# Kernel optimization log

Measured on AMD Instinct MI355X. Metric: run time of the kernel, lower is better.

## Reference

```python
import jax, jax.numpy as jnp
import numpy as np

KERNEL_SIZE = 3
IGNORE_INDEX = -100


def _unfold(x, k):
    """nn.Unfold(kernel_size=k), stride=1, no padding.
    x: (n, c, h, w) -> (n, c, k*k, L) with L=(h-k+1)*(w-k+1),
    kernel positions in row-major order (matches torch)."""
    n, c, h, w = x.shape
    hp, wp = h - k + 1, w - k + 1
    patches = jnp.stack(
        [x[:, :, i:i + hp, j:j + wp] for i in range(k) for j in range(k)],
        axis=2)  # (n, c, k*k, hp, wp)
    return patches.reshape(n, c, k * k, hp * wp)


def setup_inputs() -> dict:
    key = jax.random.key(0)
    k1, k2 = jax.random.split(key)
    logits = jax.random.normal(k1, (2, 19, 384, 384), dtype=jnp.float32)
    labels = jax.random.randint(k2, (2, 384, 384), 0, 19, dtype=jnp.int32)
    return {"logits": logits, "labels": labels}


def reference(logits, labels):
    n, c, h, w = logits.shape
    # convert_to_one_hot with ignore_index -> zero vector at ignored pixels
    valid = (labels != IGNORE_INDEX)
    oh = jax.nn.one_hot(jnp.where(valid, labels, 0), c, dtype=logits.dtype)
    oh = oh * valid[..., None].astype(logits.dtype)
    oh = jnp.transpose(oh, (0, 3, 1, 2))  # (n, c, h, w)

    lu = _unfold(logits, KERNEL_SIZE)  # (n, c, 9, L)
    yu = _unfold(oh, KERNEL_SIZE)      # (n, c, 9, L)

    aff_map = jnp.einsum('ncal,ncbl->nabl', lu, lu)  # pairwise logit affinity
    lb_map = jnp.einsum('ncal,ncbl->nabl', yu, yu)   # pairwise label affinity

    # BCEWithLogitsLoss(reduction='mean'), numerically stable form
    x, y = aff_map, lb_map
    loss = jnp.mean(jnp.maximum(x, 0) - x * y + jnp.log1p(jnp.exp(-jnp.abs(x))))
    return loss
```

## Files before the change

### kernel.cpp

```cpp
#include <hip/hip_runtime.h>


#define IGNORE_INDEX (-100)

constexpr int Hh = 384, Ww = 384, Cc = 19;
constexpr int HW = Hh * Ww;
constexpr int HP = 382, WP = 382;
constexpr int TX = 32, TY = 8;
constexpr int NT = TX * TY;
constexpr int LXX = TX + 4;
constexpr int LYY = TY + 2;
constexpr int CS  = 20;
constexpr int NBX = Ww / TX, NBY = Hh / TY;
constexpr int NBLK = NBX * NBY * 2;

__device__ __forceinline__ int mult_y(int y, int di) {
    int lo = y - (HP - 1); if (lo < 0) lo = 0;
    int hi = 2 - di;       if (y < hi) hi = y;
    int c = hi - lo + 1;   return c > 0 ? c : 0;
}
__device__ __forceinline__ int mult_x(int x, int dj) {
    int lo = (-dj > 0) ? -dj : 0;
    int lo2 = x - (WP - 1); if (lo2 > lo) lo = lo2;
    int hi = (2 - dj < 2) ? (2 - dj) : 2;
    if (x < hi) hi = x;
    int c = hi - lo + 1;   return c > 0 ? c : 0;
}

__device__ __forceinline__ float softplus(float t) {
    float e = __builtin_amdgcn_exp2f(-1.4426950408889634f * fabsf(t));
    float l = __builtin_amdgcn_logf(1.0f + e);
    return fmaxf(t, 0.0f) + 0.6931471805599453f * l;
}

__global__ __launch_bounds__(NT, 4) void aff_loss_kernel(
        const float* __restrict__ logits, const int* __restrict__ labels,
        double* __restrict__ partial) {
    __shared__ __align__(16) float sv[LYY * LXX * CS];
    __shared__ int   sl[LYY * LXX];
    __shared__ float sred[NT / 64];

    const int n   = blockIdx.z;
    const int tx0 = blockIdx.x * TX;
    const int ty0 = blockIdx.y * TY;
    const int tid = threadIdx.x;
    const int bid = (blockIdx.z * NBY + blockIdx.y) * NBX + blockIdx.x;

    const float* img = logits + (size_t)n * Cc * HW;
    const int*   lab = labels + (size_t)n * HW;

    for (int idx = tid; idx < LYY * LXX; idx += NT) {
        int r = idx / LXX, col = idx - r * LXX;
        int gy = ty0 + r;       if (gy > Hh - 1) gy = Hh - 1;
        int gx = tx0 + col - 2; if (gx < 0) gx = 0; if (gx > Ww - 1) gx = Ww - 1;
        sl[idx] = lab[gy * Ww + gx];
        const float* s = img + gy * Ww + gx;
        float4 t0, t1, t2, t3, t4;
        t0.x = s[0 * HW];  t0.y = s[1 * HW];  t0.z = s[2 * HW];  t0.w = s[3 * HW];
        t1.x = s[4 * HW];  t1.y = s[5 * HW];  t1.z = s[6 * HW];  t1.w = s[7 * HW];
        t2.x = s[8 * HW];  t2.y = s[9 * HW];  t2.z = s[10 * HW]; t2.w = s[11 * HW];
        t3.x = s[12 * HW]; t3.y = s[13 * HW]; t3.z = s[14 * HW]; t3.w = s[15 * HW];
        t4.x = s[16 * HW]; t4.y = s[17 * HW]; t4.z = s[18 * HW]; t4.w = 0.0f;
        float4* dst = reinterpret_cast<float4*>(&sv[idx * CS]);
        dst[0] = t0; dst[1] = t1; dst[2] = t2; dst[3] = t3; dst[4] = t4;
    }
    __syncthreads();

    const int tx = tid & (TX - 1), ty = tid >> 5;
    const int x = tx0 + tx, y = ty0 + ty;
    const int ep = ty * LXX + (tx + 2);

    const float4* P = reinterpret_cast<const float4*>(&sv[ep * CS]);
    const float4 p0 = P[0], p1 = P[1], p2 = P[2], p3 = P[3], p4 = P[4];
    const int lp = sl[ep];
    const bool vp = (lp != IGNORE_INDEX);

    float myf[3], mxf[5];
    #pragma unroll
    for (int i = 0; i < 3; ++i) myf[i] = (float)mult_y(y, i);
    #pragma unroll
    for (int j = 0; j < 5; ++j) mxf[j] = (float)mult_x(x, j - 2);

    auto dot19 = [&](float4 b0, float4 b1, float4 b2, float4 b3, float4 b4) {
        float xa = p0.x * b0.x, xb = p0.y * b0.y;
        xa = fmaf(p0.z, b0.z, xa); xb = fmaf(p0.w, b0.w, xb);
        xa = fmaf(p1.x, b1.x, xa); xb = fmaf(p1.y, b1.y, xb);
        xa = fmaf(p1.z, b1.z, xa); xb = fmaf(p1.w, b1.w, xb);
        xa = fmaf(p2.x, b2.x, xa); xb = fmaf(p2.y, b2.y, xb);
        xa = fmaf(p2.z, b2.z, xa); xb = fmaf(p2.w, b2.w, xb);
        xa = fmaf(p3.x, b3.x, xa); xb = fmaf(p3.y, b3.y, xb);
        xa = fmaf(p3.z, b3.z, xa); xb = fmaf(p3.w, b3.w, xb);
        xa = fmaf(p4.x, b4.x, xa); xb = fmaf(p4.y, b4.y, xb);
        xa = fmaf(p4.z, b4.z, xa);
        return xa + xb;
    };

    float tsum;
    {
        float xd = dot19(p0, p1, p2, p3, p4);
        float t = vp ? -xd : xd;
        tsum = (myf[0] * mxf[2]) * softplus(t);
    }

    const int DY[12] = {0, 0, 1, 1, 1, 1, 1, 2, 2, 2, 2, 2};
    const int DX[12] = {1, 2, -2, -1, 0, 1, 2, -2, -1, 0, 1, 2};
    #pragma unroll
    for (int dd = 0; dd < 12; dd += 2) {
        const int dy0 = DY[dd], dx0 = DX[dd];
        const int dy1 = DY[dd + 1], dx1 = DX[dd + 1];
        const int eq0 = (ty + dy0) * LXX + (tx + 2 + dx0);
        const int eq1 = (ty + dy1) * LXX + (tx + 2 + dx1);
        const float4* Q0 = reinterpret_cast<const float4*>(&sv[eq0 * CS]);
        const float4* Q1 = reinterpret_cast<const float4*>(&sv[eq1 * CS]);
        float4 a0 = Q0[0], a1 = Q0[1], a2 = Q0[2], a3 = Q0[3], a4 = Q0[4];
        float4 c0 = Q1[0], c1 = Q1[1], c2 = Q1[2], c3 = Q1[3], c4 = Q1[4];
        const int lq0 = sl[eq0], lq1 = sl[eq1];
        const float x0 = dot19(a0, a1, a2, a3, a4);
        const float x1 = dot19(c0, c1, c2, c3, c4);
        const float t0 = (vp && lq0 == lp) ? -x0 : x0;
        const float t1 = (vp && lq1 == lp) ? -x1 : x1;
        const float w0 = 2.0f * myf[dy0] * mxf[dx0 + 2];
        const float w1 = 2.0f * myf[dy1] * mxf[dx1 + 2];
        tsum = fmaf(w0, softplus(t0), tsum);
        tsum = fmaf(w1, softplus(t1), tsum);
    }

    for (int off = 32; off > 0; off >>= 1) tsum += __shfl_down(tsum, off, 64);
    const int wid = tid >> 6;
    if ((tid & 63) == 0) sred[wid] = tsum;
    __syncthreads();
    if (tid == 0) {
        double s = 0.0;
        #pragma unroll
        for (int i = 0; i < NT / 64; ++i) s += (double)sred[i];
        partial[bid] = s;
    }
}

__global__ __launch_bounds__(256) void finalize_kernel(
        const double* __restrict__ partial, float* __restrict__ out) {
    __shared__ double sred[4];
    const int tid = threadIdx.x;
    double s = 0.0;
    for (int i = tid; i < NBLK; i += 256) s += partial[i];
    for (int off = 32; off > 0; off >>= 1) s += __shfl_down(s, off, 64);
    if ((tid & 63) == 0) sred[tid >> 6] = s;
    __syncthreads();
    if (tid == 0) {
        double tot = sred[0] + sred[1] + sred[2] + sred[3];
        out[0] = (float)(tot * (1.0 / 23639688.0));
    }
}

extern "C" void kernel_launch(void* const* d_in, const int* in_sizes, int n_in,
                              void* d_out, int out_size, void* d_ws, size_t ws_size,
                              hipStream_t stream) {
    const float* logits = (const float*)d_in[0];
    const int*   labels = (const int*)d_in[1];
    float* out = (float*)d_out;
    double* partial = (double*)d_ws;

    dim3 grid(NBX, NBY, 2);
    aff_loss_kernel<<<grid, NT, 0, stream>>>(logits, labels, partial);
    finalize_kernel<<<1, 256, 0, stream>>>(partial, out);
}
```

Measured before the change: 80.38 us.

## Repack logits into pixel-major channel-padded layout before affinity loss

Adds a repack kernel that transposes the NCHW logits through shared memory into a pixel-major layout with 20 floats per pixel in workspace. The main kernel then loads each halo pixel with five float4 reads instead of nineteen strided scalar loads. The cost is an extra pass that reads the logits and writes a larger intermediate buffer, plus a third kernel launch. It also folds the factor of two into the column multiplicity weights.

Result: slower. 89.03 us (+10.8%).

```diff
diff --git a/kernel.cpp b/kernel.cpp
--- a/kernel.cpp
+++ b/kernel.cpp
@@ -13,6 +13,9 @@
 constexpr int CS  = 20;
 constexpr int NBX = Ww / TX, NBY = Hh / TY;
 constexpr int NBLK = NBX * NBY * 2;
+
+constexpr int AY = 4, AX = 64;
+constexpr int ACS = 21;
 
 __device__ __forceinline__ int mult_y(int y, int di) {
     int lo = y - (HP - 1); if (lo < 0) lo = 0;
@@ -33,8 +36,41 @@
     return fmaxf(t, 0.0f) + 0.6931471805599453f * l;
 }
 
+__global__ __launch_bounds__(256) void repack_kernel(
+        const float* __restrict__ logits, float* __restrict__ rp) {
+    __shared__ float sA[AY * AX * ACS];
+    const int n  = blockIdx.z;
+    const int y0 = blockIdx.y * AY;
+    const int x0 = blockIdx.x * AX;
+    const int tid = threadIdx.x;
+    const float* img = logits + (size_t)n * Cc * HW;
+
+    for (int task = tid; task < Cc * AY * 16; task += 256) {
+        const int c = task >> 6;
+        const int j = task & 63;
+        const int row = j >> 4, seg = j & 15;
+        const float4 v = *reinterpret_cast<const float4*>(
+            img + ((size_t)c * Hh + (y0 + row)) * Ww + x0 + seg * 4);
+        float* d = &sA[((row * AX) + seg * 4) * ACS + c];
+        d[0 * ACS] = v.x; d[1 * ACS] = v.y; d[2 * ACS] = v.z; d[3 * ACS] = v.w;
+    }
+    __syncthreads();
+
+    const int row = tid >> 6, sx = tid & 63;
+    const float* sp = &sA[(row * AX + sx) * ACS];
+    float4 t0, t1, t2, t3, t4;
+    t0.x = sp[0];  t0.y = sp[1];  t0.z = sp[2];  t0.w = sp[3];
+    t1.x = sp[4];  t1.y = sp[5];  t1.z = sp[6];  t1.w = sp[7];
+    t2.x = sp[8];  t2.y = sp[9];  t2.z = sp[10]; t2.w = sp[11];
+    t3.x = sp[12]; t3.y = sp[13]; t3.z = sp[14]; t3.w = sp[15];
+    t4.x = sp[16]; t4.y = sp[17]; t4.z = sp[18]; t4.w = 0.0f;
+    float4* dst = reinterpret_cast<float4*>(
+        rp + ((size_t)n * HW + (size_t)(y0 + row) * Ww + (x0 + sx)) * CS);
+    dst[0] = t0; dst[1] = t1; dst[2] = t2; dst[3] = t3; dst[4] = t4;
+}
+
 __global__ __launch_bounds__(NT, 4) void aff_loss_kernel(
-        const float* __restrict__ logits, const int* __restrict__ labels,
+        const float* __restrict__ rp, const int* __restrict__ labels,
         double* __restrict__ partial) {
     __shared__ __align__(16) float sv[LYY * LXX * CS];
     __shared__ int   sl[LYY * LXX];
@@ -46,7 +82,7 @@
     const int tid = threadIdx.x;
     const int bid = (blockIdx.z * NBY + blockIdx.y) * NBX + blockIdx.x;
 
-    const float* img = logits + (size_t)n * Cc * HW;
+    const float* src = rp + (size_t)n * HW * CS;
     const int*   lab = labels + (size_t)n * HW;
 
     for (int idx = tid; idx < LYY * LXX; idx += NT) {
@@ -54,15 +90,10 @@
         int gy = ty0 + r;       if (gy > Hh - 1) gy = Hh - 1;
         int gx = tx0 + col - 2; if (gx < 0) gx = 0; if (gx > Ww - 1) gx = Ww - 1;
         sl[idx] = lab[gy * Ww + gx];
-        const float* s = img + gy * Ww + gx;
-        float4 t0, t1, t2, t3, t4;
-        t0.x = s[0 * HW];  t0.y = s[1 * HW];  t0.z = s[2 * HW];  t0.w = s[3 * HW];
-        t1.x = s[4 * HW];  t1.y = s[5 * HW];  t1.z = s[6 * HW];  t1.w = s[7 * HW];
-        t2.x = s[8 * HW];  t2.y = s[9 * HW];  t2.z = s[10 * HW]; t2.w = s[11 * HW];
-        t3.x = s[12 * HW]; t3.y = s[13 * HW]; t3.z = s[14 * HW]; t3.w = s[15 * HW];
-        t4.x = s[16 * HW]; t4.y = s[17 * HW]; t4.z = s[18 * HW]; t4.w = 0.0f;
+        const float4* s = reinterpret_cast<const float4*>(
+            src + ((size_t)gy * Ww + gx) * CS);
         float4* dst = reinterpret_cast<float4*>(&sv[idx * CS]);
-        dst[0] = t0; dst[1] = t1; dst[2] = t2; dst[3] = t3; dst[4] = t4;
+        dst[0] = s[0]; dst[1] = s[1]; dst[2] = s[2]; dst[3] = s[3]; dst[4] = s[4];
     }
     __syncthreads();
 
@@ -75,11 +106,11 @@
     const int lp = sl[ep];
     const bool vp = (lp != IGNORE_INDEX);
 
-    float myf[3], mxf[5];
+    float myf[3], mxf2[5];
     #pragma unroll
     for (int i = 0; i < 3; ++i) myf[i] = (float)mult_y(y, i);
     #pragma unroll
-    for (int j = 0; j < 5; ++j) mxf[j] = (float)mult_x(x, j - 2);
+    for (int j = 0; j < 5; ++j) mxf2[j] = 2.0f * (float)mult_x(x, j - 2);
 
     auto dot19 = [&](float4 b0, float4 b1, float4 b2, float4 b3, float4 b4) {
         float xa = p0.x * b0.x, xb = p0.y * b0.y;
@@ -99,7 +130,7 @@
     {
         float xd = dot19(p0, p1, p2, p3, p4);
         float t = vp ? -xd : xd;
-        tsum = (myf[0] * mxf[2]) * softplus(t);
+        tsum = (0.5f * myf[0] * mxf2[2]) * softplus(t);
     }
 
     const int DY[12] = {0, 0, 1, 1, 1, 1, 1, 2, 2, 2, 2, 2};
@@ -119,15 +150,12 @@
         const float x1 = dot19(c0, c1, c2, c3, c4);
         const float t0 = (vp && lq0 == lp) ? -x0 : x0;
         const float t1 = (vp && lq1 == lp) ? -x1 : x1;
-        const float w0 = 2.0f * myf[dy0] * mxf[dx0 + 2];
-        const float w1 = 2.0f * myf[dy1] * mxf[dx1 + 2];
-        tsum = fmaf(w0, softplus(t0), tsum);
-        tsum = fmaf(w1, softplus(t1), tsum);
+        tsum = fmaf(myf[dy0] * mxf2[dx0 + 2], softplus(t0), tsum);
+        tsum = fmaf(myf[dy1] * mxf2[dx1 + 2], softplus(t1), tsum);
     }
 
     for (int off = 32; off > 0; off >>= 1) tsum += __shfl_down(tsum, off, 64);
-    const int wid = tid >> 6;
-    if ((tid & 63) == 0) sred[wid] = tsum;
+    if ((tid & 63) == 0) sred[tid >> 6] = tsum;
     __syncthreads();
     if (tid == 0) {
         double s = 0.0;
@@ -158,9 +186,14 @@
     const float* logits = (const float*)d_in[0];
     const int*   labels = (const int*)d_in[1];
     float* out = (float*)d_out;
-    double* partial = (double*)d_ws;
+    float* rp = (float*)d_ws;
+    double* partial = (double*)((char*)d_ws + (32u << 20));
 
-    dim3 grid(NBX, NBY, 2);
-    aff_loss_kernel<<<grid, NT, 0, stream>>>(logits, labels, partial);
+    dim3 gridA(Ww / AX, Hh / AY, 2);
+    repack_kernel<<<gridA, 256, 0, stream>>>(logits, rp);
+
+    dim3 gridB(NBX, NBY, 2);
+    aff_loss_kernel<<<gridB, NT, 0, stream>>>(rp, labels, partial);
+
     finalize_kernel<<<1, 256, 0, stream>>>(partial, out);
 }
```

## Process both batch images per block with register-prefetched second tile

Applied to the files above, without the earlier changes.

Each block now handles the same spatial tile for both batch images. The second image's halo is loaded into registers while the first tile is computed, so global-load latency overlaps with compute. The grid is flattened and remapped with an XCD-style swizzle of block indices, and the factor of 2 is folded into the x weights. The grid shrinks by half, and each thread holds 40 extra registers for prefetch, which may reduce occupancy.

Result: faster. 74.79 us (-7.0%).

```diff
diff --git a/kernel.cpp b/kernel.cpp
--- a/kernel.cpp
+++ b/kernel.cpp
@@ -10,9 +10,10 @@
 constexpr int NT = TX * TY;
 constexpr int LXX = TX + 4;
 constexpr int LYY = TY + 2;
+constexpr int NE  = LYY * LXX;
 constexpr int CS  = 20;
 constexpr int NBX = Ww / TX, NBY = Hh / TY;
-constexpr int NBLK = NBX * NBY * 2;
+constexpr int NBLK = NBX * NBY;
 
 __device__ __forceinline__ int mult_y(int y, int di) {
     int lo = y - (HP - 1); if (lo < 0) lo = 0;
@@ -36,98 +37,123 @@
 __global__ __launch_bounds__(NT, 4) void aff_loss_kernel(
         const float* __restrict__ logits, const int* __restrict__ labels,
         double* __restrict__ partial) {
-    __shared__ __align__(16) float sv[LYY * LXX * CS];
-    __shared__ int   sl[LYY * LXX];
+    __shared__ __align__(16) float sv[NE * CS];
+    __shared__ int   sl[NE];
     __shared__ float sred[NT / 64];
 
-    const int n   = blockIdx.z;
-    const int tx0 = blockIdx.x * TX;
-    const int ty0 = blockIdx.y * TY;
+    const int bid = ((int)blockIdx.x & 7) * (NBLK / 8) + ((int)blockIdx.x >> 3);
+    const int bx = bid % NBX, by = bid / NBX;
+    const int tx0 = bx * TX, ty0 = by * TY;
     const int tid = threadIdx.x;
-    const int bid = (blockIdx.z * NBY + blockIdx.y) * NBX + blockIdx.x;
-
-    const float* img = logits + (size_t)n * Cc * HW;
-    const int*   lab = labels + (size_t)n * HW;
-
-    for (int idx = tid; idx < LYY * LXX; idx += NT) {
-        int r = idx / LXX, col = idx - r * LXX;
-        int gy = ty0 + r;       if (gy > Hh - 1) gy = Hh - 1;
-        int gx = tx0 + col - 2; if (gx < 0) gx = 0; if (gx > Ww - 1) gx = Ww - 1;
-        sl[idx] = lab[gy * Ww + gx];
-        const float* s = img + gy * Ww + gx;
-        float4 t0, t1, t2, t3, t4;
-        t0.x = s[0 * HW];  t0.y = s[1 * HW];  t0.z = s[2 * HW];  t0.w = s[3 * HW];
-        t1.x = s[4 * HW];  t1.y = s[5 * HW];  t1.z = s[6 * HW];  t1.w = s[7 * HW];
-        t2.x = s[8 * HW];  t2.y = s[9 * HW];  t2.z = s[10 * HW]; t2.w = s[11 * HW];
-        t3.x = s[12 * HW]; t3.y = s[13 * HW]; t3.z = s[14 * HW]; t3.w = s[15 * HW];
-        t4.x = s[16 * HW]; t4.y = s[17 * HW]; t4.z = s[18 * HW]; t4.w = 0.0f;
-        float4* dst = reinterpret_cast<float4*>(&sv[idx * CS]);
-        dst[0] = t0; dst[1] = t1; dst[2] = t2; dst[3] = t3; dst[4] = t4;
-    }
-    __syncthreads();
 
     const int tx = tid & (TX - 1), ty = tid >> 5;
     const int x = tx0 + tx, y = ty0 + ty;
     const int ep = ty * LXX + (tx + 2);
 
-    const float4* P = reinterpret_cast<const float4*>(&sv[ep * CS]);
-    const float4 p0 = P[0], p1 = P[1], p2 = P[2], p3 = P[3], p4 = P[4];
-    const int lp = sl[ep];
-    const bool vp = (lp != IGNORE_INDEX);
-
-    float myf[3], mxf[5];
+    float myf[3], mxf2[5];
     #pragma unroll
     for (int i = 0; i < 3; ++i) myf[i] = (float)mult_y(y, i);
     #pragma unroll
-    for (int j = 0; j < 5; ++j) mxf[j] = (float)mult_x(x, j - 2);
+    for (int j = 0; j < 5; ++j) mxf2[j] = 2.0f * (float)mult_x(x, j - 2);
 
-    auto dot19 = [&](float4 b0, float4 b1, float4 b2, float4 b3, float4 b4) {
-        float xa = p0.x * b0.x, xb = p0.y * b0.y;
-        xa = fmaf(p0.z, b0.z, xa); xb = fmaf(p0.w, b0.w, xb);
-        xa = fmaf(p1.x, b1.x, xa); xb = fmaf(p1.y, b1.y, xb);
-        xa = fmaf(p1.z, b1.z, xa); xb = fmaf(p1.w, b1.w, xb);
-        xa = fmaf(p2.x, b2.x, xa); xb = fmaf(p2.y, b2.y, xb);
-        xa = fmaf(p2.z, b2.z, xa); xb = fmaf(p2.w, b2.w, xb);
-        xa = fmaf(p3.x, b3.x, xa); xb = fmaf(p3.y, b3.y, xb);
-        xa = fmaf(p3.z, b3.z, xa); xb = fmaf(p3.w, b3.w, xb);
-        xa = fmaf(p4.x, b4.x, xa); xb = fmaf(p4.y, b4.y, xb);
-        xa = fmaf(p4.z, b4.z, xa);
-        return xa + xb;
+    const int e0 = tid, e1 = tid + NT;
+    const bool has2 = (e1 < NE);
+
+    auto load_entry = [&](const float* img, const int* lab, int idx,
+                          float v[20], int& l) {
+        int r = idx / LXX, col = idx - r * LXX;
+        int gy = ty0 + r;       if (gy > Hh - 1) gy = Hh - 1;
+        int gx = tx0 + col - 2; if (gx < 0) gx = 0; if (gx > Ww - 1) gx = Ww - 1;
+        l = lab[gy * Ww + gx];
+        const float* s = img + gy * Ww + gx;
+        #pragma unroll
+        for (int c = 0; c < 19; ++c) v[c] = s[(size_t)c * HW];
+        v[19] = 0.0f;
+    };
+    auto write_entry = [&](int idx, const float v[20], int l) {
+        sl[idx] = l;
+        float4* dst = reinterpret_cast<float4*>(&sv[idx * CS]);
+        dst[0] = make_float4(v[0],  v[1],  v[2],  v[3]);
+        dst[1] = make_float4(v[4],  v[5],  v[6],  v[7]);
+        dst[2] = make_float4(v[8],  v[9],  v[10], v[11]);
+        dst[3] = make_float4(v[12], v[13], v[14], v[15]);
+        dst[4] = make_float4(v[16], v[17], v[18], v[19]);
     };
 
-    float tsum;
-    {
-        float xd = dot19(p0, p1, p2, p3, p4);
-        float t = vp ? -xd : xd;
-        tsum = (myf[0] * mxf[2]) * softplus(t);
-    }
+    auto compute_tile = [&]() -> float {
+        const float4* P = reinterpret_cast<const float4*>(&sv[ep * CS]);
+        const float4 p0 = P[0], p1 = P[1], p2 = P[2], p3 = P[3], p4 = P[4];
+        const int lp = sl[ep];
+        const bool vp = (lp != IGNORE_INDEX);
 
-    const int DY[12] = {0, 0, 1, 1, 1, 1, 1, 2, 2, 2, 2, 2};
-    const int DX[12] = {1, 2, -2, -1, 0, 1, 2, -2, -1, 0, 1, 2};
-    #pragma unroll
-    for (int dd = 0; dd < 12; dd += 2) {
-        const int dy0 = DY[dd], dx0 = DX[dd];
-        const int dy1 = DY[dd + 1], dx1 = DX[dd + 1];
-        const int eq0 = (ty + dy0) * LXX + (tx + 2 + dx0);
-        const int eq1 = (ty + dy1) * LXX + (tx + 2 + dx1);
-        const float4* Q0 = reinterpret_cast<const float4*>(&sv[eq0 * CS]);
-        const float4* Q1 = reinterpret_cast<const float4*>(&sv[eq1 * CS]);
-        float4 a0 = Q0[0], a1 = Q0[1], a2 = Q0[2], a3 = Q0[3], a4 = Q0[4];
-        float4 c0 = Q1[0], c1 = Q1[1], c2 = Q1[2], c3 = Q1[3], c4 = Q1[4];
-        const int lq0 = sl[eq0], lq1 = sl[eq1];
-        const float x0 = dot19(a0, a1, a2, a3, a4);
-        const float x1 = dot19(c0, c1, c2, c3, c4);
-        const float t0 = (vp && lq0 == lp) ? -x0 : x0;
-        const float t1 = (vp && lq1 == lp) ? -x1 : x1;
-        const float w0 = 2.0f * myf[dy0] * mxf[dx0 + 2];
-        const float w1 = 2.0f * myf[dy1] * mxf[dx1 + 2];
-        tsum = fmaf(w0, softplus(t0), tsum);
-        tsum = fmaf(w1, softplus(t1), tsum);
-    }
+        auto dot19 = [&](float4 b0, float4 b1, float4 b2, float4 b3, float4 b4) {
+            float xa = p0.x * b0.x, xb = p0.y * b0.y;
+            xa = fmaf(p0.z, b0.z, xa); xb = fmaf(p0.w, b0.w, xb);
+            xa = fmaf(p1.x, b1.x, xa); xb = fmaf(p1.y, b1.y, xb);
+            xa = fmaf(p1.z, b1.z, xa); xb = fmaf(p1.w, b1.w, xb);
+            xa = fmaf(p2.x, b2.x, xa); xb = fmaf(p2.y, b2.y, xb);
+            xa = fmaf(p2.z, b2.z, xa); xb = fmaf(p2.w, b2.w, xb);
+            xa = fmaf(p3.x, b3.x, xa); xb = fmaf(p3.y, b3.y, xb);
+            xa = fmaf(p3.z, b3.z, xa); xb = fmaf(p3.w, b3.w, xb);
+            xa = fmaf(p4.x, b4.x, xa); xb = fmaf(p4.y, b4.y, xb);
+            xa = fmaf(p4.z, b4.z, xa);
+            return xa + xb;
+        };
+
+        float ts;
+        {
+            float xd = dot19(p0, p1, p2, p3, p4);
+            float t = vp ? -xd : xd;
+            ts = (0.5f * myf[0] * mxf2[2]) * softplus(t);
+        }
+        const int DY[12] = {0, 0, 1, 1, 1, 1, 1, 2, 2, 2, 2, 2};
+        const int DX[12] = {1, 2, -2, -1, 0, 1, 2, -2, -1, 0, 1, 2};
+        #pragma unroll
+        for (int dd = 0; dd < 12; dd += 2) {
+            const int dy0 = DY[dd], dx0 = DX[dd];
+            const int dy1 = DY[dd + 1], dx1 = DX[dd + 1];
+            const int eq0 = (ty + dy0) * LXX + (tx + 2 + dx0);
+            const int eq1 = (ty + dy1) * LXX + (tx + 2 + dx1);
+            const float4* Q0 = reinterpret_cast<const float4*>(&sv[eq0 * CS]);
+            const float4* Q1 = reinterpret_cast<const float4*>(&sv[eq1 * CS]);
+            float4 a0 = Q0[0], a1 = Q0[1], a2 = Q0[2], a3 = Q0[3], a4 = Q0[4];
+            float4 c0 = Q1[0], c1 = Q1[1], c2 = Q1[2], c3 = Q1[3], c4 = Q1[4];
+            const int lq0 = sl[eq0], lq1 = sl[eq1];
+            const float x0 = dot19(a0, a1, a2, a3, a4);
+            const float x1 = dot19(c0, c1, c2, c3, c4);
+            const float t0 = (vp && lq0 == lp) ? -x0 : x0;
+            const float t1 = (vp && lq1 == lp) ? -x1 : x1;
+            ts = fmaf(myf[dy0] * mxf2[dx0 + 2], softplus(t0), ts);
+            ts = fmaf(myf[dy1] * mxf2[dx1 + 2], softplus(t1), ts);
+        }
+        return ts;
+    };
+
+    float va[20], vb[20]; int la, lb;
+
+    load_entry(logits, labels, e0, va, la);
+    if (has2) load_entry(logits, labels, e1, vb, lb);
+    write_entry(e0, va, la);
+    if (has2) write_entry(e1, vb, lb);
+    __syncthreads();
+
+    const float* img1 = logits + (size_t)Cc * HW;
+    const int*   lab1 = labels + HW;
+    load_entry(img1, lab1, e0, va, la);
+    if (has2) load_entry(img1, lab1, e1, vb, lb);
+    __builtin_amdgcn_sched_barrier(0);
+
+    float tsum = compute_tile();
+
+    __syncthreads();
+    write_entry(e0, va, la);
+    if (has2) write_entry(e1, vb, lb);
+    __syncthreads();
+
+    tsum += compute_tile();
 
     for (int off = 32; off > 0; off >>= 1) tsum += __shfl_down(tsum, off, 64);
-    const int wid = tid >> 6;
-    if ((tid & 63) == 0) sred[wid] = tsum;
+    if ((tid & 63) == 0) sred[tid >> 6] = tsum;
     __syncthreads();
     if (tid == 0) {
         double s = 0.0;
@@ -160,7 +186,6 @@
     float* out = (float*)d_out;
     double* partial = (double*)d_ws;
 
-    dim3 grid(NBX, NBY, 2);
-    aff_loss_kernel<<<grid, NT, 0, stream>>>(logits, labels, partial);
+    aff_loss_kernel<<<dim3(NBLK), dim3(NT), 0, stream>>>(logits, labels, partial);
     finalize_kernel<<<1, 256, 0, stream>>>(partial, out);
 }
```
